# Kernel tuning notes

Measured on AMD Instinct MI355X. Metric: run time of the kernel, lower is better.

The kernel has to match this reference:

```python
import jax, jax.numpy as jnp
import numpy as np
from jax import lax

B, SQ, SK, D, K = 4, 2048, 2048, 1024, 3


def setup_inputs() -> dict:
    key = jax.random.key(0)
    ks = jax.random.split(key, 16)
    s = 0.02
    return {
        "query_hidden": jax.random.normal(ks[0], (B, SQ, D), jnp.float32),
        "memory_hidden": jax.random.normal(ks[1], (B, SK, D), jnp.float32),
        "attention_mask": jax.random.randint(ks[2], (SQ, SK), 0, 2).astype(bool),
        # Linear projections (torch: y = x @ W.T + b)
        "q_w": jax.random.normal(ks[3], (D, D), jnp.float32) * s,
        "q_b": jnp.zeros((D,), jnp.float32),
        "k_w": jax.random.normal(ks[4], (D, D), jnp.float32) * s,
        "k_b": jnp.zeros((D,), jnp.float32),
        "v_w": jax.random.normal(ks[5], (D, D), jnp.float32) * s,
        "v_b": jnp.zeros((D,), jnp.float32),
        "o_w": jax.random.normal(ks[6], (D, D), jnp.float32) * s,
        "o_b": jnp.zeros((D,), jnp.float32),
        # ConvTransform1D: depthwise conv kernels [D,1,K], bias [D], scalar gate
        "q_kernel": jax.random.normal(ks[7], (D, 1, K), jnp.float32) * s,
        "q_cbias": jnp.zeros((D,), jnp.float32),
        "q_gate": jnp.zeros((), jnp.float32),
        "k_kernel": jax.random.normal(ks[8], (D, 1, K), jnp.float32) * s,
        "k_cbias": jnp.zeros((D,), jnp.float32),
        "k_gate": jnp.zeros((), jnp.float32),
        "v_kernel": jax.random.normal(ks[9], (D, 1, K), jnp.float32) * s,
        "v_cbias": jnp.zeros((D,), jnp.float32),
        "v_gate": jnp.zeros((), jnp.float32),
    }


def _conv_transform(x, kernel, cbias, gate):
    """Gated depthwise 1D conv along seq: x + tanh(gate) * dwconv(x). x: [B,S,D]."""
    xc = jnp.transpose(x, (0, 2, 1))  # [B,D,S]
    y = lax.conv_general_dilated(
        xc, kernel, window_strides=(1,), padding="SAME",
        dimension_numbers=("NCH", "OIH", "NCH"), feature_group_count=x.shape[-1])
    y = y + cbias[None, :, None]
    return x + jnp.tanh(gate) * jnp.transpose(y, (0, 2, 1))


def reference(query_hidden, memory_hidden, attention_mask,
              q_w, q_b, k_w, k_b, v_w, v_b, o_w, o_b,
              q_kernel, q_cbias, q_gate,
              k_kernel, k_cbias, k_gate,
              v_kernel, v_cbias, v_gate):
    d_model = query_hidden.shape[-1]
    q = _conv_transform(query_hidden @ q_w.T + q_b, q_kernel, q_cbias, q_gate)
    k = _conv_transform(memory_hidden @ k_w.T + k_b, k_kernel, k_cbias, k_gate)
    v = _conv_transform(memory_hidden @ v_w.T + v_b, v_kernel, v_cbias, v_gate)
    # [B,Sq,Sk]
    logits = jnp.einsum("bqd,bkd->bqk", q, k) / jnp.sqrt(jnp.float32(d_model))
    mask = attention_mask[None, :, :]  # broadcast like torch unsqueeze(0)
    logits = jnp.where(mask, logits, jnp.finfo(logits.dtype).min)
    attn = jax.nn.softmax(logits, axis=-1)
    out = jnp.einsum("bqk,bkd->bqd", attn, v) @ o_w.T + o_b
    return out
```

## Files before the change

kernel.cpp:

```cpp
#include <hip/hip_runtime.h>
#include <cstdint>
#include <cstddef>


#define GLOBAL_AS __attribute__((address_space(1)))
#define LDS_AS    __attribute__((address_space(3)))

typedef _Float16 h8 __attribute__((ext_vector_type(8)));
typedef float    f4_t __attribute__((ext_vector_type(4)));
typedef unsigned short us8 __attribute__((ext_vector_type(8)));

__device__ __forceinline__ float bf2f(unsigned short u) {
    union { unsigned int i; float f; } x; x.i = ((unsigned int)u) << 16; return x.f;
}
__device__ __forceinline__ float rd(const void* p, long i, int isBf) {
    return isBf ? bf2f(((const unsigned short*)p)[i]) : ((const float*)p)[i];
}

struct Probe16 { const unsigned short* p[16]; int n[16]; };

__global__ void k_probes(Probe16 a, const unsigned int* __restrict__ mask,
                         int* __restrict__ flags) {
    if (blockIdx.x < 16) {
        __shared__ int cnt;
        if (threadIdx.x == 0) cnt = 0;
        __syncthreads();
        const unsigned short* s = a.p[blockIdx.x];
        const int n = a.n[blockIdx.x];
        int bad = 0;
        for (int i = threadIdx.x; i < n; i += 256) {
            int e = (s[i] >> 7) & 0xFF;
            if (e >= 0x8F || (e > 0 && e <= 0x60)) bad++;
        }
        atomicAdd(&cnt, bad);
        __syncthreads();
        if (threadIdx.x == 0) flags[blockIdx.x] = (cnt * 4 > n) ? 0 : 1;
    } else {
        __shared__ int vi32, vf32, vbf, vf16;
        if (threadIdx.x == 0) { vi32 = vf32 = vbf = vf16 = 0; }
        __syncthreads();
        int bi32 = 0, bf32 = 0, bbf = 0, bf16c = 0;
        for (int i = threadIdx.x; i < 4096; i += 256) {
            unsigned int w = mask[i];
            if (!(w == 0u || w == 1u)) bi32++;
            if (!(w == 0u || w == 0x3F800000u)) bf32++;
            unsigned int h0 = w & 0xFFFFu, h1 = w >> 16;
            if (!((h0 == 0u || h0 == 0x3F80u) && (h1 == 0u || h1 == 0x3F80u))) bbf++;
            if (!((h0 == 0u || h0 == 0x3C00u) && (h1 == 0u || h1 == 0x3C00u))) bf16c++;
        }
        if (bi32) atomicAdd(&vi32, 1);
        if (bf32) atomicAdd(&vf32, 1);
        if (bbf)  atomicAdd(&vbf, 1);
        if (bf16c) atomicAdd(&vf16, 1);
        __syncthreads();
        if (threadIdx.x == 0) {
            int w;
            if (vi32 == 0) w = 4;
            else if (vf32 == 0) w = 4;
            else if (vbf == 0) w = 2;
            else if (vf16 == 0) w = 2;
            else w = 1;
            flags[16] = w;
        }
    }
}

__global__ void k_mask_bytes(const void* __restrict__ m, unsigned char* __restrict__ out,
                             long n, const int* __restrict__ widthFlag) {
    long i = ((long)blockIdx.x * 256 + threadIdx.x) * 4;
    if (i >= n) return;
    const int w = *widthFlag;
    unsigned int packed = 0;
    if (w == 4) {
        const unsigned int* p = (const unsigned int*)m;
#pragma unroll
        for (int u = 0; u < 4; ++u) packed |= (p[i + u] != 0u ? 1u : 0u) << (8 * u);
    } else if (w == 2) {
        const unsigned short* p = (const unsigned short*)m;
#pragma unroll
        for (int u = 0; u < 4; ++u) packed |= (p[i + u] != 0u ? 1u : 0u) << (8 * u);
    } else {
        const unsigned char* p = (const unsigned char*)m;
#pragma unroll
        for (int u = 0; u < 4; ++u) packed |= (p[i + u] != 0u ? 1u : 0u) << (8 * u);
    }
    *(unsigned int*)(out + i) = packed;
}

struct ConvSrc { const void* kern[3]; const void* cb[3]; const void* gate[3]; };
__global__ void k_conv_params(ConvSrc p, const int* __restrict__ flags,
                              _Float16* __restrict__ out, float* __restrict__ tg, int D) {
#pragma unroll
    for (int t = 0; t < 3; ++t) {
        const int kIs = flags[6 + t], cIs = flags[13 + t];
        for (int d = threadIdx.x; d < D; d += 256) {
#pragma unroll
            for (int j = 0; j < 3; ++j)
                out[t * 3 * D + j * D + d] = (_Float16)rd(p.kern[t], (long)d * 3 + j, kIs);
            out[9 * D + t * D + d] = (_Float16)rd(p.cb[t], d, cIs);
        }
    }
    if (threadIdx.x < 3) {
        const void* g = p.gate[threadIdx.x];
        float gv = rd(g, 0, ((const unsigned int*)g)[0] == 0u ? 1 : 0);
        tg[threadIdx.x] = tanhf(gv);
    }
}

__device__ __forceinline__ h8 cvt8(const void* src, size_t off8, int isBf) {
    h8 d;
    if (isBf) {
        us8 s = *(const us8*)((const unsigned short*)src + off8 * 8);
#pragma unroll
        for (int u = 0; u < 8; ++u) d[u] = (_Float16)bf2f(s[u]);
    } else {
        const float* f = (const float*)src + off8 * 8;
        f4_t a = *(const f4_t*)f;
        f4_t b = *(const f4_t*)(f + 4);
#pragma unroll
        for (int u = 0; u < 4; ++u) { d[u] = (_Float16)a[u]; d[4 + u] = (_Float16)b[u]; }
    }
    return d;
}

__global__ void k_h_to_f16(const void* __restrict__ s0, const void* __restrict__ s1,
                           _Float16* __restrict__ dst, int n8each,
                           const int* __restrict__ flags) {
    int i = blockIdx.x * blockDim.x + threadIdx.x;
    if (i >= 2 * n8each) return;
    int seg = i / n8each, off = i - seg * n8each;
    h8 d = cvt8(seg ? s1 : s0, off, flags[seg]);
    *(h8*)(dst + (size_t)i * 8) = d;
}

struct Ptr4 { const void* p[4]; };
__global__ void k_w_to_f16(Ptr4 srcs, _Float16* __restrict__ dst, int n8each,
                           const int* __restrict__ flags) {
    int i = blockIdx.x * blockDim.x + threadIdx.x;
    if (i >= 4 * n8each) return;
    int seg = i / n8each, off = i - seg * n8each;
    h8 d = cvt8(srcs.p[seg], off, flags[seg]);
    *(h8*)(dst + (size_t)i * 8) = d;
}

template <int MODE, int MTILE>
__global__ __launch_bounds__(256, 4) void k_gemm_nt(
    const _Float16* __restrict__ A, const _Float16* __restrict__ Bm,
    void* __restrict__ Cout,
    const void* __restrict__ bias, const int* __restrict__ biasFlag,
    const void* __restrict__ bias2, const int* __restrict__ biasFlag2,
    int N, int K, long sA, long sB, long sC,
    float scale, const unsigned char* __restrict__ mask8,
    int NT, int BZ) {

    constexpr int NI = (MTILE == 128) ? 4 : 2;
    constexpr int NCA = MTILE / 32;
    __shared__ __align__(16) _Float16 As[MTILE * 64];
    __shared__ __align__(16) _Float16 Bs[128 * 64];

    const long id = blockIdx.x;
    const int xcd = (int)(id & 7);
    const long local = id >> 3;
    const int col = (int)(local % NT);
    const long g = (local / NT) * 8 + xcd;
    const int bz = (int)(g % BZ);
    const int brow = (int)(g / BZ);

    const int tid  = threadIdx.x;
    const int wave = tid >> 6, lane = tid & 63;
    const int wm = (wave >> 1) * (MTILE / 2), wn = (wave & 1) * 64;
    const int lr = lane & 15, lq = lane >> 4;

    const _Float16* Ab = A + (long)bz * sA + (size_t)brow * MTILE * K;
    const _Float16* Bb = Bm + (long)bz * sB + (size_t)col * 128 * K;

    f4_t acc[NI][4] = {};

    const _Float16* gA[NCA];
    _Float16* lA[NCA];
#pragma unroll
    for (int j = 0; j < NCA; ++j) {
        int c = tid + j * 256;
        int r = c >> 3, s = ((c & 7) - r) & 7;
        gA[j] = Ab + (size_t)r * K + s * 8;
        lA[j] = As + c * 8;
    }
    const _Float16* gB[4];
    _Float16* lB[4];
#pragma unroll
    for (int j = 0; j < 4; ++j) {
        int c = tid + j * 256;
        int r = c >> 3, s = ((c & 7) - r) & 7;
        gB[j] = Bb + (size_t)r * K + s * 8;
        lB[j] = Bs + c * 8;
    }

    for (int kb = 0; kb < K; kb += 64) {
#pragma unroll
        for (int j = 0; j < NCA; ++j)
            __builtin_amdgcn_global_load_lds((void GLOBAL_AS*)(gA[j] + kb), (void LDS_AS*)lA[j], 16, 0, 0);
#pragma unroll
        for (int j = 0; j < 4; ++j)
            __builtin_amdgcn_global_load_lds((void GLOBAL_AS*)(gB[j] + kb), (void LDS_AS*)lB[j], 16, 0, 0);
        __syncthreads();

#pragma unroll
        for (int t = 0; t < 2; ++t) {
            const int fs = ((t * 4 + lq + lr) & 7) * 8;
            h8 af[NI], bfr[4];
#pragma unroll
            for (int i = 0; i < NI; ++i) af[i]  = *(const h8*)&As[(wm + i * 16 + lr) * 64 + fs];
#pragma unroll
            for (int j = 0; j < 4; ++j) bfr[j] = *(const h8*)&Bs[(wn + j * 16 + lr) * 64 + fs];
#pragma unroll
            for (int i = 0; i < NI; ++i)
#pragma unroll
                for (int j = 0; j < 4; ++j)
                    acc[i][j] = __builtin_amdgcn_mfma_f32_16x16x32_f16(af[i], bfr[j], acc[i][j], 0, 0, 0);
        }
        __syncthreads();
    }

    const long row0 = (long)brow * MTILE + wm + lq * 4;
    const long col0 = (long)col * 128 + wn + lr;

    {
        float bv[4];
        if constexpr (MODE != 0) {
            const void* bp = bias; const int* bfp = biasFlag; long boff = 0;
            if (bias2 != nullptr && col * 128 >= (N >> 1)) {
                bp = bias2; bfp = biasFlag2; boff = (long)(N >> 1);
            }
            const int bIs = *bfp;
#pragma unroll
            for (int j = 0; j < 4; ++j) bv[j] = rd(bp, col0 + j * 16 - boff, bIs);
        } else {
#pragma unroll
            for (int j = 0; j < 4; ++j) bv[j] = 0.0f;
        }
        if constexpr (MODE == 2) {
            float* C = (float*)Cout + (long)bz * sC;
#pragma unroll
            for (int i = 0; i < NI; ++i)
#pragma unroll
                for (int j = 0; j < 4; ++j)
#pragma unroll
                    for (int r = 0; r < 4; ++r)
                        C[(row0 + i * 16 + r) * (long)N + col0 + j * 16] = acc[i][j][r] + bv[j];
        } else {
            _Float16* C = (_Float16*)Cout + (long)bz * sC;
#pragma unroll
            for (int i = 0; i < NI; ++i)
#pragma unroll
                for (int j = 0; j < 4; ++j)
#pragma unroll
                    for (int r = 0; r < 4; ++r) {
                        float v = acc[i][j][r] + bv[j];
                        v = fminf(fmaxf(v, -65000.0f), 65000.0f);
                        C[(row0 + i * 16 + r) * (long)N + col0 + j * 16] = (_Float16)v;
                    }
        }
    }
    (void)scale; (void)mask8;
}

template <int MODE>
__global__ __launch_bounds__(512, 2) void k_gemm16(
    const _Float16* __restrict__ A, const _Float16* __restrict__ Bm,
    void* __restrict__ Cout,
    const void* __restrict__ bias, const int* __restrict__ biasFlag,
    const void* __restrict__ bias2, const int* __restrict__ biasFlag2,
    int N, int K, long sA, long sB, long sC,
    float scale, const unsigned char* __restrict__ mask8,
    int NT, int BZ) {

    __shared__ __align__(16) _Float16 AS[2][2][8192];
    __shared__ __align__(16) _Float16 BS[2][2][8192];

    const long id = blockIdx.x;
    const int xcd = (int)(id & 7);
    const long local = id >> 3;
    const int col = (int)(local % NT);
    const long g = (local / NT) * 8 + xcd;
    const int bz = (int)(g % BZ);
    const int brow = (int)(g / BZ);

    const int tid  = threadIdx.x;
    const int wave = tid >> 6, lane = tid & 63;
    const int wr = wave >> 2, wc = wave & 3;
    const int lr = lane & 15, lq = lane >> 4;

    const _Float16* Ab = A + (long)bz * sA + (size_t)brow * 256 * K;
    const _Float16* Bb = Bm + (long)bz * sB + (size_t)col * 256 * K;

    f4_t acc[8][4] = {};

    const _Float16* gAsrc[2][2];
    const _Float16* gBsrc[2][2];
    int lOff[2];
#pragma unroll
    for (int j = 0; j < 2; ++j) {
        int c = tid + j * 512;
        int rho = c >> 3, s = ((c & 7) - rho) & 7;
        lOff[j] = c * 8;
#pragma unroll
        for (int gg = 0; gg < 2; ++gg) {
            int ra = gg * 64 + (rho & 63) + (rho >> 6) * 128;
            gAsrc[gg][j] = Ab + (size_t)ra * K + s * 8;
            int rb = gg * 32 + (rho & 31) + (rho >> 5) * 64;
            gBsrc[gg][j] = Bb + (size_t)rb * K + s * 8;
        }
    }

#define STAGE_A(buf, gg, kb)                                                              \
    do {                                                                                  \
        __builtin_amdgcn_global_load_lds((void GLOBAL_AS*)(gAsrc[gg][0] + (kb)),          \
                                         (void LDS_AS*)&AS[buf][gg][lOff[0]], 16, 0, 0);  \
        __builtin_amdgcn_global_load_lds((void GLOBAL_AS*)(gAsrc[gg][1] + (kb)),          \
                                         (void LDS_AS*)&AS[buf][gg][lOff[1]], 16, 0, 0);  \
    } while (0)
#define STAGE_B(buf, gg, kb)                                                              \
    do {                                                                                  \
        __builtin_amdgcn_global_load_lds((void GLOBAL_AS*)(gBsrc[gg][0] + (kb)),          \
                                         (void LDS_AS*)&BS[buf][gg][lOff[0]], 16, 0, 0);  \
        __builtin_amdgcn_global_load_lds((void GLOBAL_AS*)(gBsrc[gg][1] + (kb)),          \
                                         (void LDS_AS*)&BS[buf][gg][lOff[1]], 16, 0, 0);  \
    } while (0)

    const int nkt = K >> 6;

    STAGE_A(0, 0, 0);
    STAGE_B(0, 0, 0);
    STAGE_B(0, 1, 0);
    STAGE_A(0, 1, 0);
    asm volatile("s_waitcnt vmcnt(4)" ::: "memory");
    __builtin_amdgcn_s_barrier();

    int cur = 0;
    for (int t = 0; t < nkt; ++t) {
        const bool pf = (t + 1) < nkt;
        const long kb = (long)(t + 1) << 6;
        const int nx = cur ^ 1;
        h8 a0[4][2], a1[4][2], b0[2][2], b1[2][2];

#pragma unroll
        for (int ks = 0; ks < 2; ++ks) {
#pragma unroll
            for (int m = 0; m < 4; ++m) {
                int rho = wr * 64 + m * 16 + lr;
                a0[m][ks] = *(const h8*)&AS[cur][0][rho * 64 + ((ks * 4 + lq + rho) & 7) * 8];
            }
#pragma unroll
            for (int n = 0; n < 2; ++n) {
                int rho = wc * 32 + n * 16 + lr;
                b0[n][ks] = *(const h8*)&BS[cur][0][rho * 64 + ((ks * 4 + lq + rho) & 7) * 8];
            }
        }
        if (pf) STAGE_A(nx, 0, kb);
        __builtin_amdgcn_s_barrier();
        __builtin_amdgcn_s_setprio(1);
#pragma unroll
        for (int ks = 0; ks < 2; ++ks)
#pragma unroll
            for (int m = 0; m < 4; ++m)
#pragma unroll
                for (int n = 0; n < 2; ++n)
                    acc[m][n] = __builtin_amdgcn_mfma_f32_16x16x32_f16(
                        a0[m][ks], b0[n][ks], acc[m][n], 0, 0, 0);
        __builtin_amdgcn_s_setprio(0);
        if (pf) asm volatile("s_waitcnt vmcnt(4)" ::: "memory");
        else    asm volatile("s_waitcnt vmcnt(2)" ::: "memory");
        __builtin_amdgcn_s_barrier();

#pragma unroll
        for (int ks = 0; ks < 2; ++ks)
#pragma unroll
            for (int n = 0; n < 2; ++n) {
                int rho = wc * 32 + n * 16 + lr;
                b1[n][ks] = *(const h8*)&BS[cur][1][rho * 64 + ((ks * 4 + lq + rho) & 7) * 8];
            }
        if (pf) STAGE_B(nx, 0, kb);
        __builtin_amdgcn_s_barrier();
        __builtin_amdgcn_s_setprio(1);
#pragma unroll
        for (int ks = 0; ks < 2; ++ks)
#pragma unroll
            for (int m = 0; m < 4; ++m)
#pragma unroll
                for (int n = 0; n < 2; ++n)
                    acc[m][2 + n] = __builtin_amdgcn_mfma_f32_16x16x32_f16(
                        a0[m][ks], b1[n][ks], acc[m][2 + n], 0, 0, 0);
        __builtin_amdgcn_s_setprio(0);
        if (pf) asm volatile("s_waitcnt vmcnt(4)" ::: "memory");
        else    asm volatile("s_waitcnt vmcnt(0)" ::: "memory");
        __builtin_amdgcn_s_barrier();

#pragma unroll
        for (int ks = 0; ks < 2; ++ks)
#pragma unroll
            for (int m = 0; m < 4; ++m) {
                int rho = wr * 64 + m * 16 + lr;
                a1[m][ks] = *(const h8*)&AS[cur][1][rho * 64 + ((ks * 4 + lq + rho) & 7) * 8];
            }
        if (pf) STAGE_B(nx, 1, kb);
        __builtin_amdgcn_s_barrier();
        __builtin_amdgcn_s_setprio(1);
#pragma unroll
        for (int ks = 0; ks < 2; ++ks)
#pragma unroll
            for (int m = 0; m < 4; ++m)
#pragma unroll
                for (int n = 0; n < 2; ++n)
                    acc[4 + m][2 + n] = __builtin_amdgcn_mfma_f32_16x16x32_f16(
                        a1[m][ks], b1[n][ks], acc[4 + m][2 + n], 0, 0, 0);
        __builtin_amdgcn_s_setprio(0);
        __builtin_amdgcn_s_barrier();

#pragma unroll
        for (int ks = 0; ks < 2; ++ks)
#pragma unroll
            for (int n = 0; n < 2; ++n) {
                int rho = wc * 32 + n * 16 + lr;
                b0[n][ks] = *(const h8*)&BS[cur][0][rho * 64 + ((ks * 4 + lq + rho) & 7) * 8];
            }
        if (pf) STAGE_A(nx, 1, kb);
        __builtin_amdgcn_s_barrier();
        __builtin_amdgcn_s_setprio(1);
#pragma unroll
        for (int ks = 0; ks < 2; ++ks)
#pragma unroll
            for (int m = 0; m < 4; ++m)
#pragma unroll
                for (int n = 0; n < 2; ++n)
                    acc[4 + m][n] = __builtin_amdgcn_mfma_f32_16x16x32_f16(
                        a1[m][ks], b0[n][ks], acc[4 + m][n], 0, 0, 0);
        __builtin_amdgcn_s_setprio(0);
        if (pf) asm volatile("s_waitcnt vmcnt(4)" ::: "memory");
        __builtin_amdgcn_s_barrier();
        cur = nx;
    }
#undef STAGE_A
#undef STAGE_B

    const long row0 = (long)brow * 256 + wr * 128 + lq * 4;
    const long col0 = (long)col * 256 + wc * 64 + lr;

    if constexpr (MODE == 3) {
        _Float16* C = (_Float16*)Cout + (long)bz * sC;
#pragma unroll
        for (int i = 0; i < 8; ++i)
#pragma unroll
            for (int j = 0; j < 4; ++j)
#pragma unroll
                for (int r = 0; r < 4; ++r) {
                    long row = row0 + i * 16 + r;
                    long ccol = col0 + j * 16;
                    bool keep = mask8[row * (long)N + ccol] != 0;
                    float v = acc[i][j][r] * scale;
                    v = fminf(fmaxf(v, -60000.0f), 60000.0f);
                    C[row * (long)N + ccol] = (_Float16)(keep ? v : -60000.0f);
                }
    } else {
        float bv[4];
        {
            const void* bp = bias; const int* bfp = biasFlag; long boff = 0;
            if (bias2 != nullptr && col * 256 >= (N >> 1)) {
                bp = bias2; bfp = biasFlag2; boff = (long)(N >> 1);
            }
            const int bIs = *bfp;
#pragma unroll
            for (int j = 0; j < 4; ++j) bv[j] = rd(bp, col0 + j * 16 - boff, bIs);
        }
        _Float16* C = (_Float16*)Cout + (long)bz * sC;
#pragma unroll
        for (int i = 0; i < 8; ++i)
#pragma unroll
            for (int j = 0; j < 4; ++j)
#pragma unroll
                for (int r = 0; r < 4; ++r) {
                    float v = acc[i][j][r] + bv[j];
                    v = fminf(fmaxf(v, -65000.0f), 65000.0f);
                    C[(row0 + i * 16 + r) * (long)N + col0 + j * 16] = (_Float16)v;
                }
    }
}

struct ConvP {
    const _Float16* x; int xs; _Float16* y;
    const _Float16* kp; const _Float16* cb; const float* tg;
};
__global__ void k_dwconv2(ConvP p0, ConvP p1, int S, int D) {
    const ConvP& p = blockIdx.z ? p1 : p0;
    int s = blockIdx.x, b = blockIdx.y;
    int d0 = threadIdx.x * 8;
    const size_t xb = ((size_t)b * S + s) * p.xs + d0;
    const size_t yb = ((size_t)b * S + s) * D + d0;
    h8 zero;
#pragma unroll
    for (int u = 0; u < 8; ++u) zero[u] = (_Float16)0.0f;
    h8 xc = *(const h8*)(p.x + xb);
    h8 xp = (s > 0)     ? *(const h8*)(p.x + xb - p.xs) : zero;
    h8 xn = (s < S - 1) ? *(const h8*)(p.x + xb + p.xs) : zero;
    h8 k0 = *(const h8*)(p.kp + 0 * D + d0);
    h8 k1 = *(const h8*)(p.kp + 1 * D + d0);
    h8 k2 = *(const h8*)(p.kp + 2 * D + d0);
    h8 cb = *(const h8*)(p.cb + d0);
    float tg = *p.tg;
    h8 o;
#pragma unroll
    for (int u = 0; u < 8; ++u) {
        float cv = (float)xp[u] * (float)k0[u] + (float)xc[u] * (float)k1[u] +
                   (float)xn[u] * (float)k2[u] + (float)cb[u];
        float v = (float)xc[u] + tg * cv;
        o[u] = (_Float16)fminf(fmaxf(v, -65000.0f), 65000.0f);
    }
    *(h8*)(p.y + yb) = o;
}

__global__ void k_dwconv_t(const _Float16* __restrict__ x, int xs,
                           _Float16* __restrict__ vt,
                           const _Float16* __restrict__ kp,
                           const _Float16* __restrict__ cbp,
                           const float* __restrict__ tgp,
                           int SK, int D) {
    __shared__ _Float16 T[64][65];
    int b = blockIdx.z;
    int s0 = blockIdx.x * 64, d0 = blockIdx.y * 64;
    int tid = threadIdx.x;
    float tg = *tgp;
    h8 zero;
#pragma unroll
    for (int u = 0; u < 8; ++u) zero[u] = (_Float16)0.0f;
#pragma unroll
    for (int it = 0; it < 2; ++it) {
        int idx = it * 256 + tid;
        int r = idx >> 3, c = (idx & 7) * 8;
        int s = s0 + r;
        const size_t xb = ((size_t)b * SK + s) * xs + d0 + c;
        h8 xc = *(const h8*)(x + xb);
        h8 xp = (s > 0)      ? *(const h8*)(x + xb - xs) : zero;
        h8 xn = (s < SK - 1) ? *(const h8*)(x + xb + xs) : zero;
        h8 k0 = *(const h8*)(kp + 0 * D + d0 + c);
        h8 k1 = *(const h8*)(kp + 1 * D + d0 + c);
        h8 k2 = *(const h8*)(kp + 2 * D + d0 + c);
        h8 cb = *(const h8*)(cbp + d0 + c);
#pragma unroll
        for (int u = 0; u < 8; ++u) {
            float cv = (float)xp[u] * (float)k0[u] + (float)xc[u] * (float)k1[u] +
                       (float)xn[u] * (float)k2[u] + (float)cb[u];
            float v = (float)xc[u] + tg * cv;
            T[r][c + u] = (_Float16)fminf(fmaxf(v, -65000.0f), 65000.0f);
        }
    }
    __syncthreads();
#pragma unroll
    for (int it = 0; it < 2; ++it) {
        int idx = it * 256 + tid;
        int dr = idx >> 3, c = (idx & 7) * 8;
        h8 o;
#pragma unroll
        for (int u = 0; u < 8; ++u) o[u] = T[c + u][dr];
        *(h8*)(vt + ((size_t)b * D + d0 + dr) * SK + s0 + c) = o;
    }
}

__global__ __launch_bounds__(256) void k_softmax(const _Float16* __restrict__ sc,
                                                 _Float16* __restrict__ pr, int SK) {
    const long row = blockIdx.x;
    const int tid = threadIdx.x, lane = tid & 63, wave = tid >> 6;
    h8 v = *(const h8*)(sc + row * (long)SK + tid * 8);
    float f[8]; float mx = -3.0e38f;
#pragma unroll
    for (int u = 0; u < 8; ++u) { f[u] = (float)v[u]; mx = fmaxf(mx, f[u]); }
#pragma unroll
    for (int o = 32; o > 0; o >>= 1) mx = fmaxf(mx, __shfl_xor(mx, o, 64));
    __shared__ float red[8];
    if (lane == 0) red[wave] = mx;
    __syncthreads();
    mx = fmaxf(fmaxf(red[0], red[1]), fmaxf(red[2], red[3]));
    float sum = 0.0f;
#pragma unroll
    for (int u = 0; u < 8; ++u) { f[u] = __expf(f[u] - mx); sum += f[u]; }
#pragma unroll
    for (int o = 32; o > 0; o >>= 1) sum += __shfl_xor(sum, o, 64);
    if (lane == 0) red[4 + wave] = sum;
    __syncthreads();
    sum = red[4] + red[5] + red[6] + red[7];
    float inv = 1.0f / sum;
    h8 o8;
#pragma unroll
    for (int u = 0; u < 8; ++u) o8[u] = (_Float16)(f[u] * inv);
    *(h8*)(pr + row * (long)SK + tid * 8) = o8;
}

extern "C" void kernel_launch(void* const* d_in, const int* in_sizes, int n_in,
                              void* d_out, int out_size, void* d_ws, size_t ws_size,
                              hipStream_t stream) {
    const int Bn = 4, SQ = 2048, SK = 2048, D = 1024;
    const size_t nQ = (size_t)Bn * SQ * D;
    const long   nM = (long)SQ * SK;

    const void* qh = d_in[0];
    const void* mh = d_in[1];
    const void* mask = d_in[2];
    const void* q_w = d_in[3];
    const void* q_b = d_in[4];
    const void* k_w = d_in[5];
    const void* k_b = d_in[6];
    const void* v_w = d_in[7];
    const void* v_b = d_in[8];
    const void* o_w = d_in[9];
    const void* o_b = d_in[10];
    const void* q_kern = d_in[11];
    const void* q_cb   = d_in[12];
    const void* q_g    = d_in[13];
    const void* k_kern = d_in[14];
    const void* k_cb   = d_in[15];
    const void* k_g    = d_in[16];
    const void* v_kern = d_in[17];
    const void* v_cb   = d_in[18];
    const void* v_g    = d_in[19];

    char* ws = (char*)d_ws;
    _Float16* scores   = (_Float16*)(ws + 0);
    _Float16* attn_out = (_Float16*)(ws + 0);
    _Float16* w16      = (_Float16*)(ws + 33554432);
    unsigned char* mask8 = (unsigned char*)(ws + 33554432);
    _Float16* par16    = (_Float16*)(ws + 37748736);
    float*    tgf      = (float*)(ws + 37748736 + 12 * 1024 * 2);
    _Float16* lin      = (_Float16*)(ws + 41943040);
    _Float16* lin_q    = lin;
    _Float16* lin_kv   = lin + nQ;
    _Float16* probs    = lin;
    _Float16* conv     = (_Float16*)(ws + 92274688);
    _Float16* qh16     = conv;
    _Float16* mh16     = conv + nQ;
    _Float16* vt       = (_Float16*)(ws + 125829120);
    int*      flags    = (int*)(ws + 142606336);

    Probe16 pa;
    const void* pp[16] = {qh, mh, q_w, k_w, v_w, o_w, q_kern, k_kern, v_kern,
                          q_b, k_b, v_b, o_b, q_cb, k_cb, v_cb};
    const int   pn[16] = {2048, 2048, 2048, 2048, 2048, 2048, 3072, 3072, 3072,
                          1024, 1024, 1024, 1024, 1024, 1024, 1024};
    for (int i = 0; i < 16; ++i) { pa.p[i] = (const unsigned short*)pp[i]; pa.n[i] = pn[i]; }
    k_probes<<<17, 256, 0, stream>>>(pa, (const unsigned int*)mask, flags);

    const int nH8 = (int)(nQ / 8);
    k_h_to_f16<<<(2 * nH8 + 255) / 256, 256, 0, stream>>>(qh, mh, qh16, nH8, flags + 0);
    const int nW8 = D * D / 8;
    Ptr4 wp; wp.p[0] = q_w; wp.p[1] = k_w; wp.p[2] = v_w; wp.p[3] = o_w;
    k_w_to_f16<<<(4 * nW8 + 255) / 256, 256, 0, stream>>>(wp, w16, nW8, flags + 2);

    k_gemm_nt<1, 64><<<dim3(1024), 256, 0, stream>>>(
        qh16, w16, lin_q, q_b, flags + 9, nullptr, nullptr,
        D, D, 0, 0, 0, 1.0f, nullptr, 8, 1);
    k_gemm16<1><<<dim3(256), 512, 0, stream>>>(
        mh16, w16 + (size_t)D * D, lin_kv, k_b, flags + 10, v_b, flags + 11,
        2 * D, D, 0, 0, 0, 1.0f, nullptr, 8, 1);

    k_mask_bytes<<<(int)(nM / 4 / 256), 256, 0, stream>>>(mask, mask8, nM, flags + 16);
    ConvSrc cs;
    cs.kern[0] = q_kern; cs.kern[1] = k_kern; cs.kern[2] = v_kern;
    cs.cb[0] = q_cb; cs.cb[1] = k_cb; cs.cb[2] = v_cb;
    cs.gate[0] = q_g; cs.gate[1] = k_g; cs.gate[2] = v_g;
    k_conv_params<<<1, 256, 0, stream>>>(cs, flags, par16, tgf, D);

    ConvP cq{lin_q, D, conv + 0 * nQ, par16 + 0 * 3 * D, par16 + 9 * D + 0 * D, tgf + 0};
    ConvP ck{lin_kv, 2 * D, conv + 1 * nQ, par16 + 1 * 3 * D, par16 + 9 * D + 1 * D, tgf + 1};
    k_dwconv2<<<dim3(SQ, Bn, 2), 128, 0, stream>>>(cq, ck, SQ, D);
    k_dwconv_t<<<dim3(SK / 64, D / 64, Bn), 256, 0, stream>>>(
        lin_kv + D, 2 * D, vt, par16 + 2 * 3 * D, par16 + 9 * D + 2 * D, tgf + 2, SK, D);

    k_gemm16<3><<<dim3(256), 512, 0, stream>>>(
        conv + 0 * nQ, conv + 1 * nQ, scores, nullptr, nullptr, nullptr, nullptr,
        SK, D, (long)SQ * D, (long)SK * D, (long)SQ * SK, 0.03125f, mask8, 8, 4);

    k_softmax<<<Bn * SQ, 256, 0, stream>>>(scores, probs, SK);

    k_gemm_nt<0, 64><<<dim3(1024), 256, 0, stream>>>(
        probs, vt, attn_out, nullptr, nullptr, nullptr, nullptr,
        D, SK, (long)SQ * SK, (long)D * SK, (long)SQ * D, 1.0f, nullptr, 8, 4);

    k_gemm_nt<2, 64><<<dim3(1024), 256, 0, stream>>>(
        attn_out, w16 + 3 * (size_t)D * D, d_out, o_b, flags + 12, nullptr, nullptr,
        D, D, 0, 0, 0, 1.0f, nullptr, 8, 1);

    (void)in_sizes; (void)n_in; (void)out_size; (void)ws_size;
}
```

Baseline: 411.1 us.

## Merge prep and conv launches, read raw mask directly in score GEMM epilogue

Combines the hidden-state and weight f16 conversion kernels into one launch, and the q/k depthwise conv and v conv-transpose kernels into one launch. It also drops the separate mask-to-bytes pass, so the score GEMM epilogue reads the raw mask using a width flag. This cuts kernel launches and one full mask read and write, but the epilogue now does a runtime-width branch and wider mask loads (up to 4 bytes per element).

```diff
diff --git a/kernel.cpp b/kernel.cpp
--- a/kernel.cpp
+++ b/kernel.cpp
@@ -65,48 +65,6 @@
     }
 }
 
-__global__ void k_mask_bytes(const void* __restrict__ m, unsigned char* __restrict__ out,
-                             long n, const int* __restrict__ widthFlag) {
-    long i = ((long)blockIdx.x * 256 + threadIdx.x) * 4;
-    if (i >= n) return;
-    const int w = *widthFlag;
-    unsigned int packed = 0;
-    if (w == 4) {
-        const unsigned int* p = (const unsigned int*)m;
-#pragma unroll
-        for (int u = 0; u < 4; ++u) packed |= (p[i + u] != 0u ? 1u : 0u) << (8 * u);
-    } else if (w == 2) {
-        const unsigned short* p = (const unsigned short*)m;
-#pragma unroll
-        for (int u = 0; u < 4; ++u) packed |= (p[i + u] != 0u ? 1u : 0u) << (8 * u);
-    } else {
-        const unsigned char* p = (const unsigned char*)m;
-#pragma unroll
-        for (int u = 0; u < 4; ++u) packed |= (p[i + u] != 0u ? 1u : 0u) << (8 * u);
-    }
-    *(unsigned int*)(out + i) = packed;
-}
-
-struct ConvSrc { const void* kern[3]; const void* cb[3]; const void* gate[3]; };
-__global__ void k_conv_params(ConvSrc p, const int* __restrict__ flags,
-                              _Float16* __restrict__ out, float* __restrict__ tg, int D) {
-#pragma unroll
-    for (int t = 0; t < 3; ++t) {
-        const int kIs = flags[6 + t], cIs = flags[13 + t];
-        for (int d = threadIdx.x; d < D; d += 256) {
-#pragma unroll
-            for (int j = 0; j < 3; ++j)
-                out[t * 3 * D + j * D + d] = (_Float16)rd(p.kern[t], (long)d * 3 + j, kIs);
-            out[9 * D + t * D + d] = (_Float16)rd(p.cb[t], d, cIs);
-        }
-    }
-    if (threadIdx.x < 3) {
-        const void* g = p.gate[threadIdx.x];
-        float gv = rd(g, 0, ((const unsigned int*)g)[0] == 0u ? 1 : 0);
-        tg[threadIdx.x] = tanhf(gv);
-    }
-}
-
 __device__ __forceinline__ h8 cvt8(const void* src, size_t off8, int isBf) {
     h8 d;
     if (isBf) {
@@ -123,24 +81,44 @@
     return d;
 }
 
-__global__ void k_h_to_f16(const void* __restrict__ s0, const void* __restrict__ s1,
-                           _Float16* __restrict__ dst, int n8each,
-                           const int* __restrict__ flags) {
-    int i = blockIdx.x * blockDim.x + threadIdx.x;
-    if (i >= 2 * n8each) return;
-    int seg = i / n8each, off = i - seg * n8each;
-    h8 d = cvt8(seg ? s1 : s0, off, flags[seg]);
-    *(h8*)(dst + (size_t)i * 8) = d;
-}
-
 struct Ptr4 { const void* p[4]; };
-__global__ void k_w_to_f16(Ptr4 srcs, _Float16* __restrict__ dst, int n8each,
-                           const int* __restrict__ flags) {
-    int i = blockIdx.x * blockDim.x + threadIdx.x;
-    if (i >= 4 * n8each) return;
-    int seg = i / n8each, off = i - seg * n8each;
-    h8 d = cvt8(srcs.p[seg], off, flags[seg]);
-    *(h8*)(dst + (size_t)i * 8) = d;
+
+__global__ void k_prep(const void* __restrict__ qh, const void* __restrict__ mh,
+                       _Float16* __restrict__ h16dst,
+                       Ptr4 wsrc, _Float16* __restrict__ w16dst,
+                       const int* __restrict__ flags) {
+    const int bid = blockIdx.x, tid = threadIdx.x;
+    if (bid < 8192) {
+        int i = bid * 256 + tid;
+        int seg = i >> 20, off = i & 1048575;
+        h8 d = cvt8(seg ? mh : qh, off, flags[seg]);
+        *(h8*)(h16dst + (size_t)i * 8) = d;
+    } else {
+        int i = (bid - 8192) * 256 + tid;
+        int seg = i >> 17, off = i & 131071;
+        h8 d = cvt8(wsrc.p[seg], off, flags[2 + seg]);
+        *(h8*)(w16dst + (size_t)i * 8) = d;
+    }
+}
+
+struct ConvSrc { const void* kern[3]; const void* cb[3]; const void* gate[3]; };
+__global__ void k_conv_params(ConvSrc p, const int* __restrict__ flags,
+                              _Float16* __restrict__ out, float* __restrict__ tg, int D) {
+#pragma unroll
+    for (int t = 0; t < 3; ++t) {
+        const int kIs = flags[6 + t], cIs = flags[13 + t];
+        for (int d = threadIdx.x; d < D; d += 256) {
+#pragma unroll
+            for (int j = 0; j < 3; ++j)
+                out[t * 3 * D + j * D + d] = (_Float16)rd(p.kern[t], (long)d * 3 + j, kIs);
+            out[9 * D + t * D + d] = (_Float16)rd(p.cb[t], d, cIs);
+        }
+    }
+    if (threadIdx.x < 3) {
+        const void* g = p.gate[threadIdx.x];
+        float gv = rd(g, 0, ((const unsigned int*)g)[0] == 0u ? 1 : 0);
+        tg[threadIdx.x] = tanhf(gv);
+    }
 }
 
 template <int MODE, int MTILE>
@@ -150,7 +128,6 @@
     const void* __restrict__ bias, const int* __restrict__ biasFlag,
     const void* __restrict__ bias2, const int* __restrict__ biasFlag2,
     int N, int K, long sA, long sB, long sC,
-    float scale, const unsigned char* __restrict__ mask8,
     int NT, int BZ) {
 
     constexpr int NI = (MTILE == 128) ? 4 : 2;
@@ -224,44 +201,41 @@
     const long row0 = (long)brow * MTILE + wm + lq * 4;
     const long col0 = (long)col * 128 + wn + lr;
 
-    {
-        float bv[4];
-        if constexpr (MODE != 0) {
-            const void* bp = bias; const int* bfp = biasFlag; long boff = 0;
-            if (bias2 != nullptr && col * 128 >= (N >> 1)) {
-                bp = bias2; bfp = biasFlag2; boff = (long)(N >> 1);
-            }
-            const int bIs = *bfp;
-#pragma unroll
-            for (int j = 0; j < 4; ++j) bv[j] = rd(bp, col0 + j * 16 - boff, bIs);
-        } else {
-#pragma unroll
-            for (int j = 0; j < 4; ++j) bv[j] = 0.0f;
-        }
-        if constexpr (MODE == 2) {
-            float* C = (float*)Cout + (long)bz * sC;
-#pragma unroll
-            for (int i = 0; i < NI; ++i)
-#pragma unroll
-                for (int j = 0; j < 4; ++j)
-#pragma unroll
-                    for (int r = 0; r < 4; ++r)
-                        C[(row0 + i * 16 + r) * (long)N + col0 + j * 16] = acc[i][j][r] + bv[j];
-        } else {
-            _Float16* C = (_Float16*)Cout + (long)bz * sC;
-#pragma unroll
-            for (int i = 0; i < NI; ++i)
-#pragma unroll
-                for (int j = 0; j < 4; ++j)
-#pragma unroll
-                    for (int r = 0; r < 4; ++r) {
-                        float v = acc[i][j][r] + bv[j];
-                        v = fminf(fmaxf(v, -65000.0f), 65000.0f);
-                        C[(row0 + i * 16 + r) * (long)N + col0 + j * 16] = (_Float16)v;
-                    }
-        }
-    }
-    (void)scale; (void)mask8;
+    float bv[4];
+    if constexpr (MODE != 0) {
+        const void* bp = bias; const int* bfp = biasFlag; long boff = 0;
+        if (bias2 != nullptr && col * 128 >= (N >> 1)) {
+            bp = bias2; bfp = biasFlag2; boff = (long)(N >> 1);
+        }
+        const int bIs = *bfp;
+#pragma unroll
+        for (int j = 0; j < 4; ++j) bv[j] = rd(bp, col0 + j * 16 - boff, bIs);
+    } else {
+#pragma unroll
+        for (int j = 0; j < 4; ++j) bv[j] = 0.0f;
+    }
+    if constexpr (MODE == 2) {
+        float* C = (float*)Cout + (long)bz * sC;
+#pragma unroll
+        for (int i = 0; i < NI; ++i)
+#pragma unroll
+            for (int j = 0; j < 4; ++j)
+#pragma unroll
+                for (int r = 0; r < 4; ++r)
+                    C[(row0 + i * 16 + r) * (long)N + col0 + j * 16] = acc[i][j][r] + bv[j];
+    } else {
+        _Float16* C = (_Float16*)Cout + (long)bz * sC;
+#pragma unroll
+        for (int i = 0; i < NI; ++i)
+#pragma unroll
+            for (int j = 0; j < 4; ++j)
+#pragma unroll
+                for (int r = 0; r < 4; ++r) {
+                    float v = acc[i][j][r] + bv[j];
+                    v = fminf(fmaxf(v, -65000.0f), 65000.0f);
+                    C[(row0 + i * 16 + r) * (long)N + col0 + j * 16] = (_Float16)v;
+                }
+    }
 }
 
 template <int MODE>
@@ -271,7 +245,7 @@
     const void* __restrict__ bias, const int* __restrict__ biasFlag,
     const void* __restrict__ bias2, const int* __restrict__ biasFlag2,
     int N, int K, long sA, long sB, long sC,
-    float scale, const unsigned char* __restrict__ mask8,
+    float scale, const void* __restrict__ mraw, const int* __restrict__ mwf,
     int NT, int BZ) {
 
     __shared__ __align__(16) _Float16 AS[2][2][8192];
@@ -446,6 +420,7 @@
     const long col0 = (long)col * 256 + wc * 64 + lr;
 
     if constexpr (MODE == 3) {
+        const int mw = *mwf;
         _Float16* C = (_Float16*)Cout + (long)bz * sC;
 #pragma unroll
         for (int i = 0; i < 8; ++i)
@@ -455,7 +430,11 @@
                 for (int r = 0; r < 4; ++r) {
                     long row = row0 + i * 16 + r;
                     long ccol = col0 + j * 16;
-                    bool keep = mask8[row * (long)N + ccol] != 0;
+                    long mi = row * (long)N + ccol;
+                    bool keep;
+                    if (mw == 4)      keep = ((const unsigned int*)mraw)[mi] != 0u;
+                    else if (mw == 2) keep = ((const unsigned short*)mraw)[mi] != 0;
+                    else              keep = ((const unsigned char*)mraw)[mi] != 0;
                     float v = acc[i][j][r] * scale;
                     v = fminf(fmaxf(v, -60000.0f), 60000.0f);
                     C[row * (long)N + ccol] = (_Float16)(keep ? v : -60000.0f);
@@ -489,78 +468,80 @@
     const _Float16* x; int xs; _Float16* y;
     const _Float16* kp; const _Float16* cb; const float* tg;
 };
-__global__ void k_dwconv2(ConvP p0, ConvP p1, int S, int D) {
-    const ConvP& p = blockIdx.z ? p1 : p0;
-    int s = blockIdx.x, b = blockIdx.y;
-    int d0 = threadIdx.x * 8;
-    const size_t xb = ((size_t)b * S + s) * p.xs + d0;
-    const size_t yb = ((size_t)b * S + s) * D + d0;
+__global__ void k_convs(ConvP p0, ConvP p1,
+                        const _Float16* __restrict__ xv, int xvs,
+                        _Float16* __restrict__ vt,
+                        const _Float16* __restrict__ kpv,
+                        const _Float16* __restrict__ cbv,
+                        const float* __restrict__ tgv,
+                        int S, int SK, int D) {
+    __shared__ _Float16 T[64][65];
+    const int bid = blockIdx.x, tid = threadIdx.x;
     h8 zero;
 #pragma unroll
     for (int u = 0; u < 8; ++u) zero[u] = (_Float16)0.0f;
-    h8 xc = *(const h8*)(p.x + xb);
-    h8 xp = (s > 0)     ? *(const h8*)(p.x + xb - p.xs) : zero;
-    h8 xn = (s < S - 1) ? *(const h8*)(p.x + xb + p.xs) : zero;
-    h8 k0 = *(const h8*)(p.kp + 0 * D + d0);
-    h8 k1 = *(const h8*)(p.kp + 1 * D + d0);
-    h8 k2 = *(const h8*)(p.kp + 2 * D + d0);
-    h8 cb = *(const h8*)(p.cb + d0);
-    float tg = *p.tg;
-    h8 o;
-#pragma unroll
-    for (int u = 0; u < 8; ++u) {
-        float cv = (float)xp[u] * (float)k0[u] + (float)xc[u] * (float)k1[u] +
-                   (float)xn[u] * (float)k2[u] + (float)cb[u];
-        float v = (float)xc[u] + tg * cv;
-        o[u] = (_Float16)fminf(fmaxf(v, -65000.0f), 65000.0f);
-    }
-    *(h8*)(p.y + yb) = o;
-}
-
-__global__ void k_dwconv_t(const _Float16* __restrict__ x, int xs,
-                           _Float16* __restrict__ vt,
-                           const _Float16* __restrict__ kp,
-                           const _Float16* __restrict__ cbp,
-                           const float* __restrict__ tgp,
-                           int SK, int D) {
-    __shared__ _Float16 T[64][65];
-    int b = blockIdx.z;
-    int s0 = blockIdx.x * 64, d0 = blockIdx.y * 64;
-    int tid = threadIdx.x;
-    float tg = *tgp;
-    h8 zero;
-#pragma unroll
-    for (int u = 0; u < 8; ++u) zero[u] = (_Float16)0.0f;
-#pragma unroll
-    for (int it = 0; it < 2; ++it) {
-        int idx = it * 256 + tid;
-        int r = idx >> 3, c = (idx & 7) * 8;
-        int s = s0 + r;
-        const size_t xb = ((size_t)b * SK + s) * xs + d0 + c;
-        h8 xc = *(const h8*)(x + xb);
-        h8 xp = (s > 0)      ? *(const h8*)(x + xb - xs) : zero;
-        h8 xn = (s < SK - 1) ? *(const h8*)(x + xb + xs) : zero;
-        h8 k0 = *(const h8*)(kp + 0 * D + d0 + c);
-        h8 k1 = *(const h8*)(kp + 1 * D + d0 + c);
-        h8 k2 = *(const h8*)(kp + 2 * D + d0 + c);
-        h8 cb = *(const h8*)(cbp + d0 + c);
+
+    if (bid < 8192) {
+        const ConvP& p = (bid >= 4096) ? p1 : p0;
+        int l = bid & 4095;
+        int b = l >> 10, sp = l & 1023;
+        int s = sp * 2 + (tid >> 7);
+        int d0 = (tid & 127) * 8;
+        const size_t xb = ((size_t)b * S + s) * p.xs + d0;
+        const size_t yb = ((size_t)b * S + s) * D + d0;
+        h8 xc = *(const h8*)(p.x + xb);
+        h8 xp = (s > 0)     ? *(const h8*)(p.x + xb - p.xs) : zero;
+        h8 xn = (s < S - 1) ? *(const h8*)(p.x + xb + p.xs) : zero;
+        h8 k0 = *(const h8*)(p.kp + 0 * D + d0);
+        h8 k1 = *(const h8*)(p.kp + 1 * D + d0);
+        h8 k2 = *(const h8*)(p.kp + 2 * D + d0);
+        h8 cb = *(const h8*)(p.cb + d0);
+        float tg = *p.tg;
+        h8 o;
 #pragma unroll
         for (int u = 0; u < 8; ++u) {
             float cv = (float)xp[u] * (float)k0[u] + (float)xc[u] * (float)k1[u] +
                        (float)xn[u] * (float)k2[u] + (float)cb[u];
             float v = (float)xc[u] + tg * cv;
-            T[r][c + u] = (_Float16)fminf(fmaxf(v, -65000.0f), 65000.0f);
-        }
-    }
-    __syncthreads();
-#pragma unroll
-    for (int it = 0; it < 2; ++it) {
-        int idx = it * 256 + tid;
-        int dr = idx >> 3, c = (idx & 7) * 8;
-        h8 o;
-#pragma unroll
-        for (int u = 0; u < 8; ++u) o[u] = T[c + u][dr];
-        *(h8*)(vt + ((size_t)b * D + d0 + dr) * SK + s0 + c) = o;
+            o[u] = (_Float16)fminf(fmaxf(v, -65000.0f), 65000.0f);
+        }
+        *(h8*)(p.y + yb) = o;
+    } else {
+        int l = bid - 8192;
+        int bx = l & 31, by = (l >> 5) & 15, b = l >> 9;
+        int s0 = bx * 64, d0 = by * 64;
+        float tg = *tgv;
+#pragma unroll
+        for (int it = 0; it < 2; ++it) {
+            int idx = it * 256 + tid;
+            int r = idx >> 3, c = (idx & 7) * 8;
+            int s = s0 + r;
+            const size_t xb = ((size_t)b * SK + s) * xvs + d0 + c;
+            h8 xc = *(const h8*)(xv + xb);
+            h8 xp = (s > 0)      ? *(const h8*)(xv + xb - xvs) : zero;
+            h8 xn = (s < SK - 1) ? *(const h8*)(xv + xb + xvs) : zero;
+            h8 k0 = *(const h8*)(kpv + 0 * D + d0 + c);
+            h8 k1 = *(const h8*)(kpv + 1 * D + d0 + c);
+            h8 k2 = *(const h8*)(kpv + 2 * D + d0 + c);
+            h8 cb = *(const h8*)(cbv + d0 + c);
+#pragma unroll
+            for (int u = 0; u < 8; ++u) {
+                float cv = (float)xp[u] * (float)k0[u] + (float)xc[u] * (float)k1[u] +
+                           (float)xn[u] * (float)k2[u] + (float)cb[u];
+                float v = (float)xc[u] + tg * cv;
+                T[r][c + u] = (_Float16)fminf(fmaxf(v, -65000.0f), 65000.0f);
+            }
+        }
+        __syncthreads();
+#pragma unroll
+        for (int it = 0; it < 2; ++it) {
+            int idx = it * 256 + tid;
+            int dr = idx >> 3, c = (idx & 7) * 8;
+            h8 o;
+#pragma unroll
+            for (int u = 0; u < 8; ++u) o[u] = T[c + u][dr];
+            *(h8*)(vt + ((size_t)b * D + d0 + dr) * SK + s0 + c) = o;
+        }
     }
 }
 
@@ -598,7 +579,6 @@
                               hipStream_t stream) {
     const int Bn = 4, SQ = 2048, SK = 2048, D = 1024;
     const size_t nQ = (size_t)Bn * SQ * D;
-    const long   nM = (long)SQ * SK;
 
     const void* qh = d_in[0];
     const void* mh = d_in[1];
@@ -625,7 +605,6 @@
     _Float16* scores   = (_Float16*)(ws + 0);
     _Float16* attn_out = (_Float16*)(ws + 0);
     _Float16* w16      = (_Float16*)(ws + 33554432);
-    unsigned char* mask8 = (unsigned char*)(ws + 33554432);
     _Float16* par16    = (_Float16*)(ws + 37748736);
     float*    tgf      = (float*)(ws + 37748736 + 12 * 1024 * 2);
     _Float16* lin      = (_Float16*)(ws + 41943040);
@@ -646,20 +625,16 @@
     for (int i = 0; i < 16; ++i) { pa.p[i] = (const unsigned short*)pp[i]; pa.n[i] = pn[i]; }
     k_probes<<<17, 256, 0, stream>>>(pa, (const unsigned int*)mask, flags);
 
-    const int nH8 = (int)(nQ / 8);
-    k_h_to_f16<<<(2 * nH8 + 255) / 256, 256, 0, stream>>>(qh, mh, qh16, nH8, flags + 0);
-    const int nW8 = D * D / 8;
     Ptr4 wp; wp.p[0] = q_w; wp.p[1] = k_w; wp.p[2] = v_w; wp.p[3] = o_w;
-    k_w_to_f16<<<(4 * nW8 + 255) / 256, 256, 0, stream>>>(wp, w16, nW8, flags + 2);
+    k_prep<<<10240, 256, 0, stream>>>(qh, mh, qh16, wp, w16, flags);
 
     k_gemm_nt<1, 64><<<dim3(1024), 256, 0, stream>>>(
         qh16, w16, lin_q, q_b, flags + 9, nullptr, nullptr,
-        D, D, 0, 0, 0, 1.0f, nullptr, 8, 1);
+        D, D, 0, 0, 0, 8, 1);
     k_gemm16<1><<<dim3(256), 512, 0, stream>>>(
         mh16, w16 + (size_t)D * D, lin_kv, k_b, flags + 10, v_b, flags + 11,
-        2 * D, D, 0, 0, 0, 1.0f, nullptr, 8, 1);
-
-    k_mask_bytes<<<(int)(nM / 4 / 256), 256, 0, stream>>>(mask, mask8, nM, flags + 16);
+        2 * D, D, 0, 0, 0, 1.0f, nullptr, nullptr, 8, 1);
+
     ConvSrc cs;
     cs.kern[0] = q_kern; cs.kern[1] = k_kern; cs.kern[2] = v_kern;
     cs.cb[0] = q_cb; cs.cb[1] = k_cb; cs.cb[2] = v_cb;
@@ -668,23 +643,23 @@
 
     ConvP cq{lin_q, D, conv + 0 * nQ, par16 + 0 * 3 * D, par16 + 9 * D + 0 * D, tgf + 0};
     ConvP ck{lin_kv, 2 * D, conv + 1 * nQ, par16 + 1 * 3 * D, par16 + 9 * D + 1 * D, tgf + 1};
-    k_dwconv2<<<dim3(SQ, Bn, 2), 128, 0, stream>>>(cq, ck, SQ, D);
-    k_dwconv_t<<<dim3(SK / 64, D / 64, Bn), 256, 0, stream>>>(
-        lin_kv + D, 2 * D, vt, par16 + 2 * 3 * D, par16 + 9 * D + 2 * D, tgf + 2, SK, D);
+    k_convs<<<dim3(10240), 256, 0, stream>>>(
+        cq, ck, lin_kv + D, 2 * D, vt, par16 + 2 * 3 * D, par16 + 9 * D + 2 * D, tgf + 2,
+        SQ, SK, D);
 
     k_gemm16<3><<<dim3(256), 512, 0, stream>>>(
         conv + 0 * nQ, conv + 1 * nQ, scores, nullptr, nullptr, nullptr, nullptr,
-        SK, D, (long)SQ * D, (long)SK * D, (long)SQ * SK, 0.03125f, mask8, 8, 4);
+        SK, D, (long)SQ * D, (long)SK * D, (long)SQ * SK, 0.03125f, mask, flags + 16, 8, 4);
 
     k_softmax<<<Bn * SQ, 256, 0, stream>>>(scores, probs, SK);
 
     k_gemm_nt<0, 64><<<dim3(1024), 256, 0, stream>>>(
         probs, vt, attn_out, nullptr, nullptr, nullptr, nullptr,
-        D, SK, (long)SQ * SK, (long)D * SK, (long)SQ * D, 1.0f, nullptr, 8, 4);
+        D, SK, (long)SQ * SK, (long)D * SK, (long)SQ * D, 8, 4);
 
     k_gemm_nt<2, 64><<<dim3(1024), 256, 0, stream>>>(
         attn_out, w16 + 3 * (size_t)D * D, d_out, o_b, flags + 12, nullptr, nullptr,
-        D, D, 0, 0, 0, 1.0f, nullptr, 8, 1);
+        D, D, 0, 0, 0, 8, 1);
 
     (void)in_sizes; (void)n_in; (void)out_size; (void)ws_size;
 }
```

Measured after the change: 444.9 us. +8.2%, slower.
